# Performance work log

Hardware: AMD Instinct MI355X
Metric: run time of the kernel (lower is better)

## Reference

```python
import jax, jax.numpy as jnp
import numpy as np

TEMPERATURE = 0.2

def setup_inputs() -> dict:
    key = jax.random.key(0)
    k1, k2 = jax.random.split(key)
    B, D = 4096, 128
    emb_i = jax.random.normal(k1, (B, D), dtype=jnp.float32)
    emb_j = jax.random.normal(k2, (B, D), dtype=jnp.float32)
    return {"emb_i": emb_i, "emb_j": emb_j}

def reference(emb_i, emb_j):
    # L2-normalize each embedding row, concat -> z: [2B, D]
    z_i = emb_i / jnp.linalg.norm(emb_i, axis=1, keepdims=True)
    z_j = emb_j / jnp.linalg.norm(emb_j, axis=1, keepdims=True)
    z = jnp.concatenate([z_i, z_j], axis=0)          # [2B, D]
    N2 = z.shape[0]
    N = N2 // 2
    # cosine similarity of normalized vectors == dot product
    sim = z @ z.T                                    # [2B, 2B]
    logits = sim / TEMPERATURE
    # denominator excludes only the diagonal (k != i)
    diag_mask = jnp.eye(N2, dtype=bool)
    masked = jnp.where(diag_mask, -jnp.inf, logits)
    lse = jax.nn.logsumexp(masked, axis=1)           # [2B]
    # positive pair for row i is i+N (mod 2N)
    pos_idx = jnp.concatenate([jnp.arange(N) + N, jnp.arange(N)])
    pos_logits = jnp.take_along_axis(logits, pos_idx[:, None], axis=1)[:, 0]
    # loss = (1/2N) * sum_i -log( exp(pos_i) / sum_{k!=i} exp(logits[i,k]) )
    loss = jnp.mean(lse - pos_logits)
    return loss
```

## Files before the change

kernel.cpp:

```cpp
#include <hip/hip_runtime.h>
#include <hip/hip_bf16.h>
#include <hip/hip_fp8.h>

typedef __attribute__((ext_vector_type(4))) float f32x4;
typedef long long i64;

#define EXP_SCALE 7.213475204444817f

__device__ __forceinline__ float fast_exp2(float x) {
#if __has_builtin(__builtin_amdgcn_exp2f)
  return __builtin_amdgcn_exp2f(x);
#else
  return exp2f(x);
#endif
}


__global__ __launch_bounds__(256) void k_normalize(
    const float* __restrict__ emb_i, const float* __restrict__ emb_j,
    unsigned char* __restrict__ z, float* __restrict__ out)
{
  if (blockIdx.x == 0 && threadIdx.x == 0) out[0] = 0.0f;
  const int t = threadIdx.x;
  const int c = t >> 4;
  const int sub = t & 15;
  const int row = (blockIdx.x << 4) + c;
  const float* src = (row < 4096) ? (emb_i + row * 128) : (emb_j + (row - 4096) * 128);
  float4 v0 = reinterpret_cast<const float4*>(src)[sub * 2];
  float4 v1 = reinterpret_cast<const float4*>(src)[sub * 2 + 1];
  float ss = v0.x*v0.x + v0.y*v0.y + v0.z*v0.z + v0.w*v0.w
           + v1.x*v1.x + v1.y*v1.y + v1.z*v1.z + v1.w*v1.w;
  #pragma unroll
  for (int m = 1; m < 16; m <<= 1) ss += __shfl_xor(ss, m, 64);
  float rinv = 1.0f / sqrtf(ss);
  unsigned char st[8];
  st[0] = __hip_fp8_e4m3(v0.x * rinv).__x;
  st[1] = __hip_fp8_e4m3(v0.y * rinv).__x;
  st[2] = __hip_fp8_e4m3(v0.z * rinv).__x;
  st[3] = __hip_fp8_e4m3(v0.w * rinv).__x;
  st[4] = __hip_fp8_e4m3(v1.x * rinv).__x;
  st[5] = __hip_fp8_e4m3(v1.y * rinv).__x;
  st[6] = __hip_fp8_e4m3(v1.z * rinv).__x;
  st[7] = __hip_fp8_e4m3(v1.w * rinv).__x;
  unsigned char* dst = z + blockIdx.x * 2048 + (sub >> 2) * 512 +
                       (((sub & 3) << 4) + c) * 8;
  *reinterpret_cast<i64*>(dst) = *reinterpret_cast<i64*>(st);
}

__global__ __launch_bounds__(512, 4) void k_simlse(
    const unsigned char* __restrict__ z,
    float* __restrict__ rpart,
    float* __restrict__ cpart,
    float* __restrict__ rowpos)
{
  const int w = threadIdx.x >> 6;
  const int g = w >> 2;
  const int cw = w & 3;
  const int lane = threadIdx.x & 63;
  const int q = lane >> 4;
  const int c = lane & 15;
  const int bid = blockIdx.x;

  int ch = (int)((sqrtf((float)(1 + 2 * bid)) - 1.0f) * 0.5f);
  if (bid >= 2 * (ch + 1) * (ch + 2)) ++ch;
  else if (bid < 2 * ch * (ch + 1)) --ch;
  const int rb = bid - 2 * ch * (ch + 1);
  const int R0 = rb << 7;
  const bool upper = (rb < (ch << 2));

  i64 a[4][4];
  {
    const unsigned char* ap = z + ((R0 >> 4) + (g << 2)) * 2048 + (lane << 3);
    #pragma unroll
    for (int rg = 0; rg < 4; ++rg)
      #pragma unroll
      for (int kk = 0; kk < 4; ++kk)
        a[rg][kk] = *reinterpret_cast<const i64*>(ap + rg * 2048 + kk * 512);
  }

  float acc[4][4];
  #pragma unroll
  for (int rg = 0; rg < 4; ++rg)
    #pragma unroll
    for (int e = 0; e < 4; ++e) acc[rg][e] = 0.0f;
  float pacc[4] = {0.f, 0.f, 0.f, 0.f};
  float colp[8];
  #pragma unroll
  for (int i = 0; i < 8; ++i) colp[i] = 0.0f;

  __shared__ float lsum[8][64];
  __shared__ float lpos[8][16];

  const int ct0 = (ch << 5) + cw;
  const unsigned char* bwave = z + ct0 * 2048 + (lane << 3);

  const int pos0t = ((R0 + (g << 6) + 4096) & 8191) >> 4;
  const int ipb = ((pos0t >> 5) == ch) ? ((pos0t & 31) >> 2) : -99;

  i64 b0[4], b1[4];
  auto ldb = [&](i64 (&dst)[4], int idx) {
    const unsigned char* p = bwave + idx * 8192;
    dst[0] = *reinterpret_cast<const i64*>(p);
    dst[1] = *reinterpret_cast<const i64*>(p + 512);
    dst[2] = *reinterpret_cast<const i64*>(p + 1024);
    dst[3] = *reinterpret_cast<const i64*>(p + 1536);
  };

  auto process = [&](const i64 (&bb)[4], int i) {
    f32x4 cc[4];
    #pragma unroll
    for (int rr = 0; rr < 4; ++rr) cc[rr] = f32x4{0.f, 0.f, 0.f, 0.f};
    #pragma unroll
    for (int kk = 0; kk < 4; ++kk)
      #pragma unroll
      for (int rr = 0; rr < 4; ++rr)
        cc[rr] = __builtin_amdgcn_mfma_f32_16x16x32_fp8_fp8(
            a[rr][kk], bb[kk], cc[rr], 0, 0, 0);
    float cp0 = 0.0f, cp1 = 0.0f;
    #pragma unroll
    for (int rr = 0; rr < 4; ++rr)
      #pragma unroll
      for (int e = 0; e < 4; ++e) {
        float tv = fast_exp2(__builtin_fmaf(cc[rr][e], EXP_SCALE, -EXP_SCALE));
        acc[rr][e] += tv;
        if (upper) { if (rr & 1) cp1 += tv; else cp0 += tv; }
      }
    if (upper) colp[i] = cp0 + cp1;
    if (i == ipb) {
      #pragma unroll
      for (int rr = 0; rr < 4; ++rr) {
        if (rr == cw) {
          #pragma unroll
          for (int e = 0; e < 4; ++e)
            if (c == ((q << 2) + e)) pacc[e] = cc[rr][e] * 5.0f;
        }
      }
    }
  };

  ldb(b0, 0);
  #pragma unroll 1
  for (int i = 0; i < 8; i += 2) {
    ldb(b1, i + 1);
    process(b0, i);
    if (i + 2 < 8) ldb(b0, i + 2);
    process(b1, i + 1);
  }

  if (upper) {
    const int cbase = 2048 * ch * (ch - 1) + (rb << 10) + (g << 9);
    #pragma unroll
    for (int j = 0; j < 8; ++j) {
      float v = colp[j];
      v += __shfl_xor(v, 16, 64);
      v += __shfl_xor(v, 32, 64);
      if (lane < 16)
        cpart[cbase + ((cw + (j << 2)) << 4) + c] = v;
    }
  }

  #pragma unroll
  for (int m = 1; m < 16; m <<= 1) {
    #pragma unroll
    for (int rg = 0; rg < 4; ++rg)
      #pragma unroll
      for (int e = 0; e < 4; ++e)
        acc[rg][e] += __shfl_xor(acc[rg][e], m, 64);
    #pragma unroll
    for (int e = 0; e < 4; ++e) pacc[e] += __shfl_xor(pacc[e], m, 64);
  }

  if (c == 0) {
    #pragma unroll
    for (int rg = 0; rg < 4; ++rg)
      #pragma unroll
      for (int e = 0; e < 4; ++e)
        lsum[w][rg * 16 + (q << 2) + e] = acc[rg][e];
    #pragma unroll
    for (int e = 0; e < 4; ++e) lpos[w][(q << 2) + e] = pacc[e];
  }
  __syncthreads();

  if (threadIdx.x < 128) {
    const int t = threadIdx.x;
    const int gg = t >> 6, tr = t & 63;
    float s = lsum[(gg << 2) + 0][tr] + lsum[(gg << 2) + 1][tr]
            + lsum[(gg << 2) + 2][tr] + lsum[(gg << 2) + 3][tr];
    rpart[(ch << 13) + R0 + t] = s;
    const bool haspos = (((((R0 + 4096) & 8191) >> 4) >> 5) == ch);
    if (haspos)
      rowpos[R0 + t] = lpos[(gg << 2) + (tr >> 4)][t & 15];
  }
}

__global__ __launch_bounds__(256) void k_finish(
    const float* __restrict__ rpart, const float* __restrict__ cpart,
    const float* __restrict__ rowpos, float* __restrict__ out)
{
  const int r = blockIdx.x * 256 + threadIdx.x;
  const int chr = r >> 9;

  float rs = 0.0f;
  #pragma unroll 4
  for (int ch = chr; ch < 16; ++ch) rs += rpart[(ch << 13) + r];

  const int nv = chr << 3;
  const float* cb = cpart + 2048 * chr * (chr - 1) + (r & 511);
  float cs0 = 0.f, cs1 = 0.f, cs2 = 0.f, cs3 = 0.f;
  #pragma unroll 2
  for (int k = 0; k < nv; k += 4) {
    cs0 += cb[(k + 0) << 9];
    cs1 += cb[(k + 1) << 9];
    cs2 += cb[(k + 2) << 9];
    cs3 += cb[(k + 3) << 9];
  }

  float tot = rs + ((cs0 + cs1) + (cs2 + cs3)) - 1.0f;
  float v = 5.0f + logf(tot) - rowpos[r & 4095];
  #pragma unroll
  for (int m = 1; m < 64; m <<= 1) v += __shfl_xor(v, m, 64);
  __shared__ float red[4];
  if ((threadIdx.x & 63) == 0) red[threadIdx.x >> 6] = v;
  __syncthreads();
  if (threadIdx.x == 0)
    atomicAdd(out, (red[0] + red[1] + red[2] + red[3]) * (1.0f / 8192.0f));
}

extern "C" void kernel_launch(void* const* d_in, const int* in_sizes, int n_in,
                              void* d_out, int out_size, void* d_ws, size_t ws_size,
                              hipStream_t stream) {
  const float* emb_i = (const float*)d_in[0];
  const float* emb_j = (const float*)d_in[1];
  unsigned char* z = (unsigned char*)d_ws;
  float* rpart = (float*)((char*)d_ws + (1 << 20));
  float* cpart = (float*)((char*)d_ws + 1572864);
  float* rowpos = (float*)((char*)d_ws + 3538944);
  float* out = (float*)d_out;

  k_normalize<<<512, 256, 0, stream>>>(emb_i, emb_j, z, out);
  k_simlse<<<544, 512, 0, stream>>>(z, rpart, cpart, rowpos);
  k_finish<<<32, 256, 0, stream>>>(rpart, cpart, rowpos, out);
}
```

Baseline: 81.82 us.

## Stage A and B fp8 tiles in LDS with 1024-thread blocks over 256-row tiles

Each block now covers 256 rows instead of 128, using 16 waves (1024 threads). It also copies the needed A rows and the 512-column B chunk (96 KB) into shared memory before computing, and all waves read their fragments from LDS instead of global/L2. The aim is to share B-tile loads across more row groups and halve the block count, which cuts redundant global traffic. In exchange it adds a blocking preload barrier with no overlap, raises LDS use per block so occupancy drops, and leaves only 272 blocks, which may not fill 256 CUs evenly.

```diff
diff --git a/kernel.cpp b/kernel.cpp
--- a/kernel.cpp
+++ b/kernel.cpp
@@ -47,7 +47,7 @@
   *reinterpret_cast<i64*>(dst) = *reinterpret_cast<i64*>(st);
 }
 
-__global__ __launch_bounds__(512, 4) void k_simlse(
+__global__ __launch_bounds__(1024, 4) void k_simlse(
     const unsigned char* __restrict__ z,
     float* __restrict__ rpart,
     float* __restrict__ cpart,
@@ -61,22 +61,35 @@
   const int c = lane & 15;
   const int bid = blockIdx.x;
 
-  int ch = (int)((sqrtf((float)(1 + 2 * bid)) - 1.0f) * 0.5f);
-  if (bid >= 2 * (ch + 1) * (ch + 2)) ++ch;
-  else if (bid < 2 * ch * (ch + 1)) --ch;
-  const int rb = bid - 2 * ch * (ch + 1);
-  const int R0 = rb << 7;
-  const bool upper = (rb < (ch << 2));
+  int ch = (int)((sqrtf((float)(4 * bid + 1)) - 1.0f) * 0.5f);
+  if (bid >= (ch + 1) * (ch + 2)) ++ch;
+  else if (bid < ch * (ch + 1)) --ch;
+  const int rb = bid - ch * (ch + 1);
+  const int R0 = rb << 8;
+  const bool upper = (rb < (ch << 1));
+
+  __shared__ unsigned char sz[98304];
+  __shared__ float lsum[16][64];
+  __shared__ float lpos[16][16];
+  {
+    const unsigned char* zA = z + (R0 >> 4) * 2048;
+    const unsigned char* zB = z + ch * 65536;
+    #pragma unroll
+    for (int j = 0; j < 6; ++j) {
+      const int off = j * 16384 + threadIdx.x * 16;
+      const unsigned char* src = (j < 2) ? (zA + off) : (zB + (off - 32768));
+      *reinterpret_cast<int4*>(&sz[off]) = *reinterpret_cast<const int4*>(src);
+    }
+  }
+  __syncthreads();
 
   i64 a[4][4];
-  {
-    const unsigned char* ap = z + ((R0 >> 4) + (g << 2)) * 2048 + (lane << 3);
-    #pragma unroll
-    for (int rg = 0; rg < 4; ++rg)
-      #pragma unroll
-      for (int kk = 0; kk < 4; ++kk)
-        a[rg][kk] = *reinterpret_cast<const i64*>(ap + rg * 2048 + kk * 512);
-  }
+  #pragma unroll
+  for (int rg = 0; rg < 4; ++rg)
+    #pragma unroll
+    for (int kk = 0; kk < 4; ++kk)
+      a[rg][kk] = *reinterpret_cast<const i64*>(
+          sz + ((g << 2) + rg) * 2048 + kk * 512 + (lane << 3));
 
   float acc[4][4];
   #pragma unroll
@@ -88,18 +101,13 @@
   #pragma unroll
   for (int i = 0; i < 8; ++i) colp[i] = 0.0f;
 
-  __shared__ float lsum[8][64];
-  __shared__ float lpos[8][16];
-
-  const int ct0 = (ch << 5) + cw;
-  const unsigned char* bwave = z + ct0 * 2048 + (lane << 3);
-
-  const int pos0t = ((R0 + (g << 6) + 4096) & 8191) >> 4;
-  const int ipb = ((pos0t >> 5) == ch) ? ((pos0t & 31) >> 2) : -99;
+  const int pos0t = ((R0 + 4096) & 8191) >> 4;
+  const bool haspos = ((pos0t >> 5) == ch);
+  const int ipb = haspos ? ((pos0t & 31) >> 2) + g : -99;
 
   i64 b0[4], b1[4];
   auto ldb = [&](i64 (&dst)[4], int idx) {
-    const unsigned char* p = bwave + idx * 8192;
+    const unsigned char* p = sz + 32768 + (cw + (idx << 2)) * 2048 + (lane << 3);
     dst[0] = *reinterpret_cast<const i64*>(p);
     dst[1] = *reinterpret_cast<const i64*>(p + 512);
     dst[2] = *reinterpret_cast<const i64*>(p + 1024);
@@ -148,7 +156,7 @@
   }
 
   if (upper) {
-    const int cbase = 2048 * ch * (ch - 1) + (rb << 10) + (g << 9);
+    const int cbase = 2048 * ch * (ch - 1) + (((rb << 2) + g) << 9);
     #pragma unroll
     for (int j = 0; j < 8; ++j) {
       float v = colp[j];
@@ -181,15 +189,14 @@
   }
   __syncthreads();
 
-  if (threadIdx.x < 128) {
+  if (threadIdx.x < 256) {
     const int t = threadIdx.x;
     const int gg = t >> 6, tr = t & 63;
     float s = lsum[(gg << 2) + 0][tr] + lsum[(gg << 2) + 1][tr]
             + lsum[(gg << 2) + 2][tr] + lsum[(gg << 2) + 3][tr];
     rpart[(ch << 13) + R0 + t] = s;
-    const bool haspos = (((((R0 + 4096) & 8191) >> 4) >> 5) == ch);
     if (haspos)
-      rowpos[R0 + t] = lpos[(gg << 2) + (tr >> 4)][t & 15];
+      rowpos[R0 + t] = lpos[(gg << 2) + ((t >> 4) & 3)][t & 15];
   }
 }
 
@@ -238,6 +245,6 @@
   float* out = (float*)d_out;
 
   k_normalize<<<512, 256, 0, stream>>>(emb_i, emb_j, z, out);
-  k_simlse<<<544, 512, 0, stream>>>(z, rpart, cpart, rowpos);
+  k_simlse<<<272, 1024, 0, stream>>>(z, rpart, cpart, rowpos);
   k_finish<<<32, 256, 0, stream>>>(rpart, cpart, rowpos, out);
 }
```

Result: slower. 86.47 us (+5.7%).
